# Kernel tuning notes

Measured on AMD Instinct MI355X. Metric: run time of the kernel, lower is better.

The kernel has to match this reference:

```python
import jax, jax.numpy as jnp
from jax import lax
import numpy as np

B, T, V, U = 64, 2048, 256, 256
BLANK = 0
NEG = jnp.float32(-1e30)


def setup_inputs() -> dict:
    key = jax.random.key(0)
    k1, k2, k3, k4 = jax.random.split(key, 4)
    logits = jax.random.normal(k1, (B, T, V), dtype=jnp.float32)
    targets = jax.random.randint(k2, (B, U), 1, V)               # labels 1..V-1 (0 = blank)
    targets_lengths = jax.random.randint(k3, (B,), U // 2, U + 1)
    logits_lengths = jax.random.randint(k4, (B,), T // 2, T + 1)
    return dict(logits=logits, targets=targets,
                logits_lengths=logits_lengths, targets_lengths=targets_lengths)


def _ctc_forced_alignment(logp, targets, logits_lengths, targets_lengths):
    """Viterbi forced alignment over the CTC extended state graph.
    Returns per-frame best-path labels, shape [B, T] (get_alignment_3d, is_ctc=True)."""
    Bs, Ts, _ = logp.shape
    Us = targets.shape[1]
    S = 2 * Us + 1
    s_idx = jnp.arange(S)
    # extended sequence: blank, t1, blank, t2, ..., blank
    lab_pos = jnp.minimum(s_idx // 2, Us - 1)
    ext = jnp.where((s_idx % 2 == 1)[None, :], jnp.take(targets, lab_pos, axis=1), BLANK)  # [B,S]
    # emission scores em[b,t,s] = logp[b,t,ext[b,s]]
    em = jnp.take_along_axis(logp, jnp.broadcast_to(ext[:, None, :], (Bs, Ts, S)), axis=2)

    valid = s_idx[None, :] < (2 * targets_lengths[:, None] + 1)              # [B,S]
    ext_m2 = jnp.pad(ext[:, :-2], ((0, 0), (2, 0)), constant_values=BLANK)
    skip_ok = (s_idx[None, :] >= 2) & ((s_idx % 2 == 1)[None, :]) & (ext != ext_m2)

    idx_blank = 2 * targets_lengths          # last blank state (S_b - 1)
    idx_label = 2 * targets_lengths - 1      # last label state (S_b - 2)

    alpha0 = jnp.where(valid & (s_idx[None, :] <= 1), em[:, 0, :], NEG)

    def pair_of(alpha):
        vb = jnp.take_along_axis(alpha, idx_blank[:, None], axis=1)
        vl = jnp.take_along_axis(alpha, idx_label[:, None], axis=1)
        return jnp.concatenate([vb, vl], axis=1)  # [B,2]

    def step(alpha, em_t):
        a1 = jnp.pad(alpha[:, :-1], ((0, 0), (1, 0)), constant_values=NEG)
        a2 = jnp.where(skip_ok, jnp.pad(alpha[:, :-2], ((0, 0), (2, 0)), constant_values=NEG), NEG)
        stacked = jnp.stack([alpha, a1, a2])     # [3,B,S]
        bp = jnp.argmax(stacked, axis=0).astype(jnp.int32)
        alpha_new = jnp.where(valid, jnp.max(stacked, axis=0) + em_t, NEG)
        return alpha_new, (bp, pair_of(alpha_new))

    _, (bps, pairs) = lax.scan(step, alpha0, jnp.moveaxis(em, 1, 0)[1:])
    bps = jnp.concatenate([jnp.zeros((1, Bs, S), jnp.int32), bps])            # [T,B,S]
    pairs = jnp.concatenate([pair_of(alpha0)[None], pairs])                   # [T,B,2]

    last_pair = pairs[logits_lengths - 1, jnp.arange(Bs)]                     # value at final valid frame
    end_state = jnp.where(last_pair[:, 0] >= last_pair[:, 1], idx_blank, idx_label).astype(jnp.int32)

    def back(s, inp):
        t, bp_t = inp
        label = jnp.take_along_axis(ext, s[:, None], axis=1)[:, 0]
        step_bp = jnp.take_along_axis(bp_t, s[:, None], axis=1)[:, 0]
        s_prev = jnp.where(t - 1 >= logits_lengths - 1, end_state, s - step_bp)
        return s_prev.astype(jnp.int32), label

    ts = jnp.arange(Ts - 1, -1, -1)
    _, labels_rev = lax.scan(back, end_state, (ts, bps[::-1]))
    return labels_rev[::-1].T  # [B,T] per-frame aligned target labels


def reference(logits, targets, logits_lengths, targets_lengths):
    logp = jax.nn.log_softmax(logits, axis=2)                                 # [B,T,V]
    aligned = lax.stop_gradient(
        _ctc_forced_alignment(logp, targets, logits_lengths, targets_lengths))
    nll = -jnp.take_along_axis(logp, aligned[:, :, None], axis=2)[..., 0]     # [B,T]
    mask = (jnp.arange(logp.shape[1])[None, :] < logits_lengths[:, None]).astype(logp.dtype)
    # reduce=True: mean over valid (unmasked) positions
    return jnp.sum(nll * mask) / jnp.sum(mask)
```

## Files before the change

kernel.cpp:

```cpp
#include <hip/hip_runtime.h>

#define NEGF -1e30f
typedef unsigned int uint32;

static constexpr int Bb = 64, Tt = 2048, Vv = 256, Uu = 256;

__device__ __forceinline__ unsigned short f2bf(float f) {
  uint32 u = __builtin_bit_cast(uint32, f);
  u += 0x7fffu + ((u >> 16) & 1u);
  return (unsigned short)(u >> 16);
}
__device__ __forceinline__ float bf2f_lo(uint32 p) { return __builtin_bit_cast(float, p << 16); }
__device__ __forceinline__ float bf2f_hi(uint32 p) { return __builtin_bit_cast(float, p & 0xffff0000u); }

__device__ __forceinline__ float dpp_shr1(float old, float src) {
  return __builtin_bit_cast(float, __builtin_amdgcn_update_dpp(
      __builtin_bit_cast(int, old), __builtin_bit_cast(int, src), 0x138, 0xF, 0xF, false));
}
__device__ __forceinline__ float dpp_shl1(float old, float src) {
  return __builtin_bit_cast(float, __builtin_amdgcn_update_dpp(
      __builtin_bit_cast(int, old), __builtin_bit_cast(int, src), 0x130, 0xF, 0xF, false));
}

__global__ __launch_bounds__(256) void gather_lse_kernel(
    const float* __restrict__ logits, const int* __restrict__ targets,
    const int* __restrict__ llen, float* __restrict__ acc,
    float* __restrict__ Ebs, unsigned short* __restrict__ E) {
  __shared__ __align__(16) float buf[4][8][Vv];
  __shared__ float wpart[4];
  const int b = blockIdx.x >> 5;
  const int c = blockIdx.x & 31;
  const int w = threadIdx.x >> 6;
  const int lane = threadIdx.x & 63;
  const int L = llen[b];
  const int4 lb = reinterpret_cast<const int4*>(targets + (b << 8))[lane];
  const float* __restrict__ lgb = logits + (size_t)b * (Tt * Vv);
  float lse_local = 0.f;
#pragma unroll
  for (int k = 0; k < 2; ++k) {
    const int tbase = (c << 6) + (k << 5) + w;
    if (tbase >= L) break;
    float4 v[8];
#pragma unroll
    for (int j = 0; j < 8; ++j)
      v[j] = reinterpret_cast<const float4*>(lgb + (size_t)(tbase + 4 * j) * Vv)[lane];
    float s[8];
#pragma unroll
    for (int j = 0; j < 8; ++j)
      s[j] = __expf(v[j].x) + __expf(v[j].y) + __expf(v[j].z) + __expf(v[j].w);
#pragma unroll
    for (int off = 32; off; off >>= 1) {
#pragma unroll
      for (int j = 0; j < 8; ++j) s[j] += __shfl_down(s[j], off);
    }
#pragma unroll
    for (int j = 0; j < 8; ++j)
      reinterpret_cast<float4*>(&buf[w][j][0])[lane] = v[j];
#pragma unroll
    for (int j = 0; j < 8; ++j) {
      const int t = tbase + 4 * j;
      const bool val = t < L;
      ushort4 o;
      o.x = f2bf(buf[w][j][lb.x]); o.y = f2bf(buf[w][j][lb.y]);
      o.z = f2bf(buf[w][j][lb.z]); o.w = f2bf(buf[w][j][lb.w]);
      if (val)
        reinterpret_cast<ushort4*>(E + ((size_t)((b << 11) + t)) * Vv)[lane] = o;
      if ((lane == 0) & val) {
        lse_local += __logf(s[j]);
        Ebs[(b << 11) + ((t == 0) ? 2047 : t - 1)] = v[j].x;
      }
    }
  }
  if (lane == 0) wpart[w] = lse_local;
  __syncthreads();
  if (threadIdx.x == 0)
    atomicAdd(acc, wpart[0] + wpart[1] + wpart[2] + wpart[3]);
}

#define PG 8
__global__ __launch_bounds__(128) void viterbi_kernel(
    const unsigned short* __restrict__ E, const float* __restrict__ Ebs,
    const int* __restrict__ targets, const int* __restrict__ llen,
    const int* __restrict__ tlen, float* __restrict__ acc) {
  __shared__ __align__(16) float LB[2048];
  __shared__ float Bt[520];
  const int b = blockIdx.x;
  const int lane = threadIdx.x & 63;
  const int wv = threadIdx.x >> 6;
  const int L = llen[b];
  const int tl = tlen[b];
  const int M = (L - 2) >> 1;
  const int4 lb = reinterpret_cast<const int4*>(targets + (b << 8))[lane];
  const uint2* __restrict__ Erow = reinterpret_cast<const uint2*>(E) + ((size_t)(b << 11) << 6);
  const float* __restrict__ Ebb = Ebs + (b << 11);

  {
    const float4* src = reinterpret_cast<const float4*>(Ebb);
    float4* dst = reinterpret_cast<float4*>(LB);
    for (int i = threadIdx.x; i < 512; i += 128) dst[i] = src[i];
  }
  __syncthreads();

  float a0 = NEGF, a1 = NEGF, a2 = NEGF, a3 = NEGF, a4 = NEGF,
        a5 = NEGF, a6 = NEGF, a7 = NEGF, a8 = NEGF;

  if (wv == 0) {
    const int prevw = __shfl_up(lb.w, 1);
    const bool sk0 = (lane != 0) && (lb.x != prevw);
    const bool sk1 = (lb.y != lb.x);
    const bool sk2 = (lb.z != lb.y);
    const bool sk3 = (lb.w != lb.z);
    if (lane == 0) {
      a0 = LB[2047];
      a1 = bf2f_lo((uint32)*reinterpret_cast<const unsigned short*>(E + ((size_t)(b << 11) << 8)));
    }
    uint2 pf[PG][4];
    float4 pb[PG];
    auto fetchf = [&](int slot, int k) {
      const int kk = (k > 511) ? 511 : k;
#pragma unroll
      for (int j = 0; j < 4; ++j) {
        int r = 1 + 4 * kk + j; r = (r > 2047) ? 2047 : r;
        pf[slot][j] = Erow[(size_t)(r << 6) + lane];
      }
      pb[slot] = reinterpret_cast<const float4*>(LB)[kk];
    };
    auto stepf = [&](uint2 em, float eb) {
      const float e0 = bf2f_lo(em.x), e1 = bf2f_hi(em.x);
      const float e2 = bf2f_lo(em.y), e3 = bf2f_hi(em.y);
      const float am1 = dpp_shr1(NEGF, a7);
      const float x0 = fmaxf(a0, am1) + eb;
      const float x1 = fmaxf(fmaxf(a1, a0), sk0 ? am1 : NEGF) + e0;
      const float x2 = fmaxf(a2, a1) + eb;
      const float x3 = fmaxf(fmaxf(a3, a2), sk1 ? a1 : NEGF) + e1;
      const float x4 = fmaxf(a4, a3) + eb;
      const float x5 = fmaxf(fmaxf(a5, a4), sk2 ? a3 : NEGF) + e2;
      const float x6 = fmaxf(a6, a5) + eb;
      const float x7 = fmaxf(fmaxf(a7, a6), sk3 ? a5 : NEGF) + e3;
      const float x8 = fmaxf(a8, a7) + eb;
      a0 = x0; a1 = x1; a2 = x2; a3 = x3; a4 = x4; a5 = x5; a6 = x6; a7 = x7; a8 = x8;
    };
    const int n = M, Gf = n >> 2, remf = n & 3;
#pragma unroll
    for (int s = 0; s < PG; ++s) fetchf(s, s);
    __builtin_amdgcn_sched_barrier(0);
    int g = 0;
    while (g + PG <= Gf) {
#pragma unroll
      for (int s = 0; s < PG; ++s) {
#pragma unroll
        for (int j = 0; j < 4; ++j) stepf(pf[s][j], (&pb[s].x)[j]);
        fetchf(s, g + s + PG);
        __builtin_amdgcn_sched_barrier(0);
      }
      g += PG;
    }
    const int left = Gf - g;
#pragma unroll
    for (int s = 0; s < PG; ++s) {
      if (s < left) {
#pragma unroll
        for (int j = 0; j < 4; ++j) stepf(pf[s][j], (&pb[s].x)[j]);
      }
    }
#pragma unroll
    for (int s = 0; s < PG; ++s) {
      if (s == left) {
#pragma unroll
        for (int j = 0; j < 4; ++j)
          if (j < remf) stepf(pf[s][j], (&pb[s].x)[j]);
      }
    }
  } else {
    const int nlabx = __shfl_down(lb.x, 1);
    const bool kb0 = (lb.y != lb.x);
    const bool kb1 = (lb.z != lb.y);
    const bool kb2 = (lb.w != lb.z);
    const bool kb3 = (lane < 63) && (nlabx != lb.w);
    {
      const uint2 er = Erow[(size_t)((L - 1) << 6) + lane];
      const float e0 = bf2f_lo(er.x), e1 = bf2f_hi(er.x);
      const float e2 = bf2f_lo(er.y), e3 = bf2f_hi(er.y);
      const float blankL = LB[L - 2];
      const int s0 = 8 * lane, tb = 2 * tl, tm = 2 * tl - 1;
      a0 = (s0     == tb) ? blankL : NEGF;
      a1 = (s0 + 1 == tm) ? e0     : NEGF;
      a2 = (s0 + 2 == tb) ? blankL : NEGF;
      a3 = (s0 + 3 == tm) ? e1     : NEGF;
      a4 = (s0 + 4 == tb) ? blankL : NEGF;
      a5 = (s0 + 5 == tm) ? e2     : NEGF;
      a6 = (s0 + 6 == tb) ? blankL : NEGF;
      a7 = (s0 + 7 == tm) ? e3     : NEGF;
      a8 = ((lane == 63) && (tb == 512)) ? blankL : NEGF;
    }
    uint2 qf[PG][4];
    float qb[PG][4];
    auto fetchb = [&](int slot, int k) {
#pragma unroll
      for (int j = 0; j < 4; ++j) {
        int r = L - 2 - 4 * k - j; r = (r < 1) ? 1 : r;
        qf[slot][j] = Erow[(size_t)(r << 6) + lane];
        qb[slot][j] = LB[r - 1];
      }
    };
    auto stepb = [&](uint2 em, float eb) {
      const float e0 = bf2f_lo(em.x), e1 = bf2f_hi(em.x);
      const float e2 = bf2f_lo(em.y), e3 = bf2f_hi(em.y);
      const float bn0 = dpp_shl1(a8, a0);
      const float bn1 = dpp_shl1(NEGF, a1);
      const float y0 = fmaxf(a0, a1) + eb;
      const float y1 = fmaxf(fmaxf(a1, a2), kb0 ? a3 : NEGF) + e0;
      const float y2 = fmaxf(a2, a3) + eb;
      const float y3 = fmaxf(fmaxf(a3, a4), kb1 ? a5 : NEGF) + e1;
      const float y4 = fmaxf(a4, a5) + eb;
      const float y5 = fmaxf(fmaxf(a5, a6), kb2 ? a7 : NEGF) + e2;
      const float y6 = fmaxf(a6, a7) + eb;
      const float y7 = fmaxf(fmaxf(a7, bn0), kb3 ? bn1 : NEGF) + e3;
      const float y8 = a8 + eb;
      a0 = y0; a1 = y1; a2 = y2; a3 = y3; a4 = y4; a5 = y5; a6 = y6; a7 = y7; a8 = y8;
    };
    const int n = L - 2 - M, Gb = n >> 2, remb = n & 3;
#pragma unroll
    for (int s = 0; s < PG; ++s) fetchb(s, s);
    __builtin_amdgcn_sched_barrier(0);
    int g = 0;
    while (g + PG <= Gb) {
#pragma unroll
      for (int s = 0; s < PG; ++s) {
#pragma unroll
        for (int j = 0; j < 4; ++j) stepb(qf[s][j], qb[s][j]);
        fetchb(s, g + s + PG);
        __builtin_amdgcn_sched_barrier(0);
      }
      g += PG;
    }
    const int left = Gb - g;
#pragma unroll
    for (int s = 0; s < PG; ++s) {
      if (s < left) {
#pragma unroll
        for (int j = 0; j < 4; ++j) stepb(qf[s][j], qb[s][j]);
      }
    }
#pragma unroll
    for (int s = 0; s < PG; ++s) {
      if (s == left) {
#pragma unroll
        for (int j = 0; j < 4; ++j)
          if (j < remb) stepb(qf[s][j], qb[s][j]);
      }
    }
    Bt[8 * lane + 0] = a0; Bt[8 * lane + 1] = a1;
    Bt[8 * lane + 2] = a2; Bt[8 * lane + 3] = a3;
    Bt[8 * lane + 4] = a4; Bt[8 * lane + 5] = a5;
    Bt[8 * lane + 6] = a6; Bt[8 * lane + 7] = a7;
    if (lane == 63) Bt[512] = a8;
    if (lane == 0) { Bt[513] = NEGF; Bt[514] = NEGF; }
  }
  __syncthreads();
  if (wv == 0) {
    const int nlabx = __shfl_down(lb.x, 1);
    const bool kb0 = (lb.y != lb.x);
    const bool kb1 = (lb.z != lb.y);
    const bool kb2 = (lb.w != lb.z);
    const bool kb3 = (lane < 63) && (nlabx != lb.w);
    const int s0 = 8 * lane;
    float best;
    best =             a0 + fmaxf(Bt[s0],     Bt[s0 + 1]);
    best = fmaxf(best, a1 + fmaxf(fmaxf(Bt[s0 + 1], Bt[s0 + 2]), kb0 ? Bt[s0 + 3] : NEGF));
    best = fmaxf(best, a2 + fmaxf(Bt[s0 + 2], Bt[s0 + 3]));
    best = fmaxf(best, a3 + fmaxf(fmaxf(Bt[s0 + 3], Bt[s0 + 4]), kb1 ? Bt[s0 + 5] : NEGF));
    best = fmaxf(best, a4 + fmaxf(Bt[s0 + 4], Bt[s0 + 5]));
    best = fmaxf(best, a5 + fmaxf(fmaxf(Bt[s0 + 5], Bt[s0 + 6]), kb2 ? Bt[s0 + 7] : NEGF));
    best = fmaxf(best, a6 + fmaxf(Bt[s0 + 6], Bt[s0 + 7]));
    best = fmaxf(best, a7 + fmaxf(fmaxf(Bt[s0 + 7], Bt[s0 + 8]), kb3 ? Bt[s0 + 9] : NEGF));
    best = fmaxf(best, a8 + Bt[512]);
#pragma unroll
    for (int off = 32; off; off >>= 1) best = fmaxf(best, __shfl_down(best, off));
    if (lane == 0) atomicAdd(acc, -best);
  }
}

__global__ __launch_bounds__(64) void finalize_kernel(
    const int* __restrict__ llen, const float* __restrict__ acc,
    float* __restrict__ out) {
  int Lsum = llen[threadIdx.x];
#pragma unroll
  for (int off = 32; off; off >>= 1) Lsum += __shfl_down(Lsum, off);
  if (threadIdx.x == 0) out[0] = acc[0] / (float)Lsum;
}

extern "C" void kernel_launch(void* const* d_in, const int* in_sizes, int n_in,
                              void* d_out, int out_size, void* d_ws, size_t ws_size,
                              hipStream_t stream) {
  const float* logits  = (const float*)d_in[0];
  const int*   targets = (const int*)d_in[1];
  const int*   llen    = (const int*)d_in[2];
  const int*   tlen    = (const int*)d_in[3];
  float* out = (float*)d_out;

  float*          acc = (float*)d_ws;
  float*          Ebs = (float*)((char*)d_ws + 4096);
  unsigned short* E   = (unsigned short*)((char*)d_ws + (1u << 20));

  hipMemsetAsync(acc, 0, 16, stream);
  gather_lse_kernel<<<Bb * 32, 256, 0, stream>>>(logits, targets, llen, acc, Ebs, E);
  viterbi_kernel<<<Bb, 128, 0, stream>>>(E, Ebs, targets, llen, tlen, acc);
  finalize_kernel<<<1, 64, 0, stream>>>(llen, acc, out);
}
```

Measured before the change: 278.5 us.

## Interleave forward and backward Viterbi passes in one wavefront

The viterbi kernel previously ran the forward and backward half-passes on two separate wavefronts of a 128-thread block. Now a single 64-lane wavefront runs both, interleaving their steps in one loop so the two independent dependency chains can hide each other's ALU and DPP latency. Prefetch depth is halved to keep register use in check, and tails are handled separately for each direction. The risk is higher register pressure and a loop that runs in series for the longer of the two halves, plus leftover steps outside the joint loop.

```diff
diff --git a/kernel.cpp b/kernel.cpp
--- a/kernel.cpp
+++ b/kernel.cpp
@@ -77,16 +77,15 @@
     atomicAdd(acc, wpart[0] + wpart[1] + wpart[2] + wpart[3]);
 }
 
-#define PG 8
-__global__ __launch_bounds__(128) void viterbi_kernel(
+#define PG 4
+__global__ __launch_bounds__(64) void viterbi_kernel(
     const unsigned short* __restrict__ E, const float* __restrict__ Ebs,
     const int* __restrict__ targets, const int* __restrict__ llen,
     const int* __restrict__ tlen, float* __restrict__ acc) {
   __shared__ __align__(16) float LB[2048];
   __shared__ float Bt[520];
   const int b = blockIdx.x;
-  const int lane = threadIdx.x & 63;
-  const int wv = threadIdx.x >> 6;
+  const int lane = threadIdx.x;
   const int L = llen[b];
   const int tl = tlen[b];
   const int M = (L - 2) >> 1;
@@ -97,184 +96,198 @@
   {
     const float4* src = reinterpret_cast<const float4*>(Ebb);
     float4* dst = reinterpret_cast<float4*>(LB);
-    for (int i = threadIdx.x; i < 512; i += 128) dst[i] = src[i];
+    for (int i = lane; i < 512; i += 64) dst[i] = src[i];
   }
   __syncthreads();
 
-  float a0 = NEGF, a1 = NEGF, a2 = NEGF, a3 = NEGF, a4 = NEGF,
-        a5 = NEGF, a6 = NEGF, a7 = NEGF, a8 = NEGF;
-
-  if (wv == 0) {
-    const int prevw = __shfl_up(lb.w, 1);
-    const bool sk0 = (lane != 0) && (lb.x != prevw);
-    const bool sk1 = (lb.y != lb.x);
-    const bool sk2 = (lb.z != lb.y);
-    const bool sk3 = (lb.w != lb.z);
-    if (lane == 0) {
-      a0 = LB[2047];
-      a1 = bf2f_lo((uint32)*reinterpret_cast<const unsigned short*>(E + ((size_t)(b << 11) << 8)));
-    }
-    uint2 pf[PG][4];
-    float4 pb[PG];
-    auto fetchf = [&](int slot, int k) {
-      const int kk = (k > 511) ? 511 : k;
+  const int prevw = __shfl_up(lb.w, 1);
+  const bool sk0 = (lane != 0) && (lb.x != prevw);
+  const bool sk1 = (lb.y != lb.x);
+  const bool sk2 = (lb.z != lb.y);
+  const bool sk3 = (lb.w != lb.z);
+  const int nlabx = __shfl_down(lb.x, 1);
+  const bool kb0 = sk1;
+  const bool kb1 = sk2;
+  const bool kb2 = sk3;
+  const bool kb3 = (lane < 63) && (nlabx != lb.w);
+
+  float f0 = NEGF, f1 = NEGF, f2 = NEGF, f3 = NEGF, f4 = NEGF,
+        f5 = NEGF, f6 = NEGF, f7 = NEGF, f8 = NEGF;
+  if (lane == 0) {
+    f0 = LB[2047];
+    f1 = bf2f_lo((uint32)*reinterpret_cast<const unsigned short*>(E + ((size_t)(b << 11) << 8)));
+  }
+
+  float h0, h1, h2, h3, h4, h5, h6, h7, h8;
+  {
+    const uint2 er = Erow[(size_t)((L - 1) << 6) + lane];
+    const float e0 = bf2f_lo(er.x), e1 = bf2f_hi(er.x);
+    const float e2 = bf2f_lo(er.y), e3 = bf2f_hi(er.y);
+    const float blankL = LB[L - 2];
+    const int s0 = 8 * lane, tb2 = 2 * tl, tm = 2 * tl - 1;
+    h0 = (s0     == tb2) ? blankL : NEGF;
+    h1 = (s0 + 1 == tm) ? e0     : NEGF;
+    h2 = (s0 + 2 == tb2) ? blankL : NEGF;
+    h3 = (s0 + 3 == tm) ? e1     : NEGF;
+    h4 = (s0 + 4 == tb2) ? blankL : NEGF;
+    h5 = (s0 + 5 == tm) ? e2     : NEGF;
+    h6 = (s0 + 6 == tb2) ? blankL : NEGF;
+    h7 = (s0 + 7 == tm) ? e3     : NEGF;
+    h8 = ((lane == 63) && (tb2 == 512)) ? blankL : NEGF;
+  }
+
+  uint2  pf[PG][4];  float4 pb4[PG];
+  uint2  qf[PG][4];  float  qb[PG][4];
+  auto fetchf = [&](int slot, int k) {
+    const int kk = (k > 511) ? 511 : k;
+#pragma unroll
+    for (int j = 0; j < 4; ++j) {
+      int r = 1 + 4 * kk + j; r = (r > 2047) ? 2047 : r;
+      pf[slot][j] = Erow[(size_t)(r << 6) + lane];
+    }
+    pb4[slot] = reinterpret_cast<const float4*>(LB)[kk];
+  };
+  auto fetchb = [&](int slot, int k) {
+#pragma unroll
+    for (int j = 0; j < 4; ++j) {
+      int r = L - 2 - 4 * k - j; r = (r < 1) ? 1 : r;
+      qf[slot][j] = Erow[(size_t)(r << 6) + lane];
+      qb[slot][j] = LB[r - 1];
+    }
+  };
+  auto stepf = [&](uint2 em, float eb) {
+    const float e0 = bf2f_lo(em.x), e1 = bf2f_hi(em.x);
+    const float e2 = bf2f_lo(em.y), e3 = bf2f_hi(em.y);
+    const float am1 = dpp_shr1(NEGF, f7);
+    const float x0 = fmaxf(f0, am1) + eb;
+    const float x1 = fmaxf(fmaxf(f1, f0), sk0 ? am1 : NEGF) + e0;
+    const float x2 = fmaxf(f2, f1) + eb;
+    const float x3 = fmaxf(fmaxf(f3, f2), sk1 ? f1 : NEGF) + e1;
+    const float x4 = fmaxf(f4, f3) + eb;
+    const float x5 = fmaxf(fmaxf(f5, f4), sk2 ? f3 : NEGF) + e2;
+    const float x6 = fmaxf(f6, f5) + eb;
+    const float x7 = fmaxf(fmaxf(f7, f6), sk3 ? f5 : NEGF) + e3;
+    const float x8 = fmaxf(f8, f7) + eb;
+    f0 = x0; f1 = x1; f2 = x2; f3 = x3; f4 = x4; f5 = x5; f6 = x6; f7 = x7; f8 = x8;
+  };
+  auto steph = [&](uint2 em, float eb) {
+    const float e0 = bf2f_lo(em.x), e1 = bf2f_hi(em.x);
+    const float e2 = bf2f_lo(em.y), e3 = bf2f_hi(em.y);
+    const float bn0 = dpp_shl1(h8, h0);
+    const float bn1 = dpp_shl1(NEGF, h1);
+    const float y0 = fmaxf(h0, h1) + eb;
+    const float y1 = fmaxf(fmaxf(h1, h2), kb0 ? h3 : NEGF) + e0;
+    const float y2 = fmaxf(h2, h3) + eb;
+    const float y3 = fmaxf(fmaxf(h3, h4), kb1 ? h5 : NEGF) + e1;
+    const float y4 = fmaxf(h4, h5) + eb;
+    const float y5 = fmaxf(fmaxf(h5, h6), kb2 ? h7 : NEGF) + e2;
+    const float y6 = fmaxf(h6, h7) + eb;
+    const float y7 = fmaxf(fmaxf(h7, bn0), kb3 ? bn1 : NEGF) + e3;
+    const float y8 = h8 + eb;
+    h0 = y0; h1 = y1; h2 = y2; h3 = y3; h4 = y4; h5 = y5; h6 = y6; h7 = y7; h8 = y8;
+  };
+
+  const int nf = M, nb = L - 2 - M;
+  const int Gf = nf >> 2, remf = nf & 3;
+  const int Gb = nb >> 2, remb = nb & 3;
+  const int Gmin = (Gf < Gb) ? Gf : Gb;
+
+#pragma unroll
+  for (int s = 0; s < PG; ++s) { fetchf(s, s); fetchb(s, s); }
+  __builtin_amdgcn_sched_barrier(0);
+
+  int g = 0;
+  while (g + PG <= Gmin) {
+#pragma unroll
+    for (int s = 0; s < PG; ++s) {
 #pragma unroll
       for (int j = 0; j < 4; ++j) {
-        int r = 1 + 4 * kk + j; r = (r > 2047) ? 2047 : r;
-        pf[slot][j] = Erow[(size_t)(r << 6) + lane];
-      }
-      pb[slot] = reinterpret_cast<const float4*>(LB)[kk];
-    };
-    auto stepf = [&](uint2 em, float eb) {
-      const float e0 = bf2f_lo(em.x), e1 = bf2f_hi(em.x);
-      const float e2 = bf2f_lo(em.y), e3 = bf2f_hi(em.y);
-      const float am1 = dpp_shr1(NEGF, a7);
-      const float x0 = fmaxf(a0, am1) + eb;
-      const float x1 = fmaxf(fmaxf(a1, a0), sk0 ? am1 : NEGF) + e0;
-      const float x2 = fmaxf(a2, a1) + eb;
-      const float x3 = fmaxf(fmaxf(a3, a2), sk1 ? a1 : NEGF) + e1;
-      const float x4 = fmaxf(a4, a3) + eb;
-      const float x5 = fmaxf(fmaxf(a5, a4), sk2 ? a3 : NEGF) + e2;
-      const float x6 = fmaxf(a6, a5) + eb;
-      const float x7 = fmaxf(fmaxf(a7, a6), sk3 ? a5 : NEGF) + e3;
-      const float x8 = fmaxf(a8, a7) + eb;
-      a0 = x0; a1 = x1; a2 = x2; a3 = x3; a4 = x4; a5 = x5; a6 = x6; a7 = x7; a8 = x8;
-    };
-    const int n = M, Gf = n >> 2, remf = n & 3;
-#pragma unroll
-    for (int s = 0; s < PG; ++s) fetchf(s, s);
-    __builtin_amdgcn_sched_barrier(0);
-    int g = 0;
-    while (g + PG <= Gf) {
+        stepf(pf[s][j], (&pb4[s].x)[j]);
+        steph(qf[s][j], qb[s][j]);
+      }
+      fetchf(s, g + s + PG);
+      fetchb(s, g + s + PG);
+      __builtin_amdgcn_sched_barrier(0);
+    }
+    g += PG;
+  }
+
+  {
+    const int leftf = Gf - g;
+#pragma unroll
+    for (int s = 0; s < PG; ++s) {
+      if (s < leftf) {
+#pragma unroll
+        for (int j = 0; j < 4; ++j) stepf(pf[s][j], (&pb4[s].x)[j]);
+      }
+    }
+    if (leftf == PG) {
+      if (remf) {
+        fetchf(0, g + PG);
+#pragma unroll
+        for (int j = 0; j < 4; ++j)
+          if (j < remf) stepf(pf[0][j], (&pb4[0].x)[j]);
+      }
+    } else {
 #pragma unroll
       for (int s = 0; s < PG; ++s) {
-#pragma unroll
-        for (int j = 0; j < 4; ++j) stepf(pf[s][j], (&pb[s].x)[j]);
-        fetchf(s, g + s + PG);
-        __builtin_amdgcn_sched_barrier(0);
-      }
-      g += PG;
-    }
-    const int left = Gf - g;
+        if (s == leftf) {
+#pragma unroll
+          for (int j = 0; j < 4; ++j)
+            if (j < remf) stepf(pf[s][j], (&pb4[s].x)[j]);
+        }
+      }
+    }
+  }
+
+  {
+    const int leftb = Gb - g;
 #pragma unroll
     for (int s = 0; s < PG; ++s) {
-      if (s < left) {
-#pragma unroll
-        for (int j = 0; j < 4; ++j) stepf(pf[s][j], (&pb[s].x)[j]);
-      }
-    }
-#pragma unroll
-    for (int s = 0; s < PG; ++s) {
-      if (s == left) {
+      if (s < leftb) {
+#pragma unroll
+        for (int j = 0; j < 4; ++j) steph(qf[s][j], qb[s][j]);
+      }
+    }
+    if (leftb == PG) {
+      if (remb) {
+        fetchb(0, g + PG);
 #pragma unroll
         for (int j = 0; j < 4; ++j)
-          if (j < remf) stepf(pf[s][j], (&pb[s].x)[j]);
-      }
-    }
-  } else {
-    const int nlabx = __shfl_down(lb.x, 1);
-    const bool kb0 = (lb.y != lb.x);
-    const bool kb1 = (lb.z != lb.y);
-    const bool kb2 = (lb.w != lb.z);
-    const bool kb3 = (lane < 63) && (nlabx != lb.w);
-    {
-      const uint2 er = Erow[(size_t)((L - 1) << 6) + lane];
-      const float e0 = bf2f_lo(er.x), e1 = bf2f_hi(er.x);
-      const float e2 = bf2f_lo(er.y), e3 = bf2f_hi(er.y);
-      const float blankL = LB[L - 2];
-      const int s0 = 8 * lane, tb = 2 * tl, tm = 2 * tl - 1;
-      a0 = (s0     == tb) ? blankL : NEGF;
-      a1 = (s0 + 1 == tm) ? e0     : NEGF;
-      a2 = (s0 + 2 == tb) ? blankL : NEGF;
-      a3 = (s0 + 3 == tm) ? e1     : NEGF;
-      a4 = (s0 + 4 == tb) ? blankL : NEGF;
-      a5 = (s0 + 5 == tm) ? e2     : NEGF;
-      a6 = (s0 + 6 == tb) ? blankL : NEGF;
-      a7 = (s0 + 7 == tm) ? e3     : NEGF;
-      a8 = ((lane == 63) && (tb == 512)) ? blankL : NEGF;
-    }
-    uint2 qf[PG][4];
-    float qb[PG][4];
-    auto fetchb = [&](int slot, int k) {
-#pragma unroll
-      for (int j = 0; j < 4; ++j) {
-        int r = L - 2 - 4 * k - j; r = (r < 1) ? 1 : r;
-        qf[slot][j] = Erow[(size_t)(r << 6) + lane];
-        qb[slot][j] = LB[r - 1];
-      }
-    };
-    auto stepb = [&](uint2 em, float eb) {
-      const float e0 = bf2f_lo(em.x), e1 = bf2f_hi(em.x);
-      const float e2 = bf2f_lo(em.y), e3 = bf2f_hi(em.y);
-      const float bn0 = dpp_shl1(a8, a0);
-      const float bn1 = dpp_shl1(NEGF, a1);
-      const float y0 = fmaxf(a0, a1) + eb;
-      const float y1 = fmaxf(fmaxf(a1, a2), kb0 ? a3 : NEGF) + e0;
-      const float y2 = fmaxf(a2, a3) + eb;
-      const float y3 = fmaxf(fmaxf(a3, a4), kb1 ? a5 : NEGF) + e1;
-      const float y4 = fmaxf(a4, a5) + eb;
-      const float y5 = fmaxf(fmaxf(a5, a6), kb2 ? a7 : NEGF) + e2;
-      const float y6 = fmaxf(a6, a7) + eb;
-      const float y7 = fmaxf(fmaxf(a7, bn0), kb3 ? bn1 : NEGF) + e3;
-      const float y8 = a8 + eb;
-      a0 = y0; a1 = y1; a2 = y2; a3 = y3; a4 = y4; a5 = y5; a6 = y6; a7 = y7; a8 = y8;
-    };
-    const int n = L - 2 - M, Gb = n >> 2, remb = n & 3;
-#pragma unroll
-    for (int s = 0; s < PG; ++s) fetchb(s, s);
-    __builtin_amdgcn_sched_barrier(0);
-    int g = 0;
-    while (g + PG <= Gb) {
+          if (j < remb) steph(qf[0][j], qb[0][j]);
+      }
+    } else {
 #pragma unroll
       for (int s = 0; s < PG; ++s) {
-#pragma unroll
-        for (int j = 0; j < 4; ++j) stepb(qf[s][j], qb[s][j]);
-        fetchb(s, g + s + PG);
-        __builtin_amdgcn_sched_barrier(0);
-      }
-      g += PG;
-    }
-    const int left = Gb - g;
-#pragma unroll
-    for (int s = 0; s < PG; ++s) {
-      if (s < left) {
-#pragma unroll
-        for (int j = 0; j < 4; ++j) stepb(qf[s][j], qb[s][j]);
-      }
-    }
-#pragma unroll
-    for (int s = 0; s < PG; ++s) {
-      if (s == left) {
-#pragma unroll
-        for (int j = 0; j < 4; ++j)
-          if (j < remb) stepb(qf[s][j], qb[s][j]);
-      }
-    }
-    Bt[8 * lane + 0] = a0; Bt[8 * lane + 1] = a1;
-    Bt[8 * lane + 2] = a2; Bt[8 * lane + 3] = a3;
-    Bt[8 * lane + 4] = a4; Bt[8 * lane + 5] = a5;
-    Bt[8 * lane + 6] = a6; Bt[8 * lane + 7] = a7;
-    if (lane == 63) Bt[512] = a8;
-    if (lane == 0) { Bt[513] = NEGF; Bt[514] = NEGF; }
-  }
+        if (s == leftb) {
+#pragma unroll
+          for (int j = 0; j < 4; ++j)
+            if (j < remb) steph(qf[s][j], qb[s][j]);
+        }
+      }
+    }
+  }
+
+  Bt[8 * lane + 0] = h0; Bt[8 * lane + 1] = h1;
+  Bt[8 * lane + 2] = h2; Bt[8 * lane + 3] = h3;
+  Bt[8 * lane + 4] = h4; Bt[8 * lane + 5] = h5;
+  Bt[8 * lane + 6] = h6; Bt[8 * lane + 7] = h7;
+  if (lane == 63) Bt[512] = h8;
+  if (lane == 0) { Bt[513] = NEGF; Bt[514] = NEGF; }
   __syncthreads();
-  if (wv == 0) {
-    const int nlabx = __shfl_down(lb.x, 1);
-    const bool kb0 = (lb.y != lb.x);
-    const bool kb1 = (lb.z != lb.y);
-    const bool kb2 = (lb.w != lb.z);
-    const bool kb3 = (lane < 63) && (nlabx != lb.w);
+
+  {
     const int s0 = 8 * lane;
     float best;
-    best =             a0 + fmaxf(Bt[s0],     Bt[s0 + 1]);
-    best = fmaxf(best, a1 + fmaxf(fmaxf(Bt[s0 + 1], Bt[s0 + 2]), kb0 ? Bt[s0 + 3] : NEGF));
-    best = fmaxf(best, a2 + fmaxf(Bt[s0 + 2], Bt[s0 + 3]));
-    best = fmaxf(best, a3 + fmaxf(fmaxf(Bt[s0 + 3], Bt[s0 + 4]), kb1 ? Bt[s0 + 5] : NEGF));
-    best = fmaxf(best, a4 + fmaxf(Bt[s0 + 4], Bt[s0 + 5]));
-    best = fmaxf(best, a5 + fmaxf(fmaxf(Bt[s0 + 5], Bt[s0 + 6]), kb2 ? Bt[s0 + 7] : NEGF));
-    best = fmaxf(best, a6 + fmaxf(Bt[s0 + 6], Bt[s0 + 7]));
-    best = fmaxf(best, a7 + fmaxf(fmaxf(Bt[s0 + 7], Bt[s0 + 8]), kb3 ? Bt[s0 + 9] : NEGF));
-    best = fmaxf(best, a8 + Bt[512]);
+    best =             f0 + fmaxf(Bt[s0],     Bt[s0 + 1]);
+    best = fmaxf(best, f1 + fmaxf(fmaxf(Bt[s0 + 1], Bt[s0 + 2]), kb0 ? Bt[s0 + 3] : NEGF));
+    best = fmaxf(best, f2 + fmaxf(Bt[s0 + 2], Bt[s0 + 3]));
+    best = fmaxf(best, f3 + fmaxf(fmaxf(Bt[s0 + 3], Bt[s0 + 4]), kb1 ? Bt[s0 + 5] : NEGF));
+    best = fmaxf(best, f4 + fmaxf(Bt[s0 + 4], Bt[s0 + 5]));
+    best = fmaxf(best, f5 + fmaxf(fmaxf(Bt[s0 + 5], Bt[s0 + 6]), kb2 ? Bt[s0 + 7] : NEGF));
+    best = fmaxf(best, f6 + fmaxf(Bt[s0 + 6], Bt[s0 + 7]));
+    best = fmaxf(best, f7 + fmaxf(fmaxf(Bt[s0 + 7], Bt[s0 + 8]), kb3 ? Bt[s0 + 9] : NEGF));
+    best = fmaxf(best, f8 + Bt[512]);
 #pragma unroll
     for (int off = 32; off; off >>= 1) best = fmaxf(best, __shfl_down(best, off));
     if (lane == 0) atomicAdd(acc, -best);
@@ -305,6 +318,6 @@
 
   hipMemsetAsync(acc, 0, 16, stream);
   gather_lse_kernel<<<Bb * 32, 256, 0, stream>>>(logits, targets, llen, acc, Ebs, E);
-  viterbi_kernel<<<Bb, 128, 0, stream>>>(E, Ebs, targets, llen, tlen, acc);
+  viterbi_kernel<<<Bb, 64, 0, stream>>>(E, Ebs, targets, llen, tlen, acc);
   finalize_kernel<<<1, 64, 0, stream>>>(llen, acc, out);
 }
```

New measurement: 340.2 us. 22.2% more time.

## Split Viterbi state range across two wavefronts per direction with wavefront-pipelined boundary exchange

Applied to the files above, without the earlier changes.

The forward and backward Viterbi passes each move from one wavefront owning 8 states per lane to two wavefronts owning 4 states per lane, one for the low half of the state range and one for the high half. The wave that depends on the other half's boundary column runs one phase of 64 frames behind, and boundary values pass through double-buffered shared memory at a barrier after each phase. This shortens the serial dependency chain per frame, roughly halving the per-step ALU work. In exchange it adds per-phase barriers, extra shared-memory traffic, and a one-phase pipeline fill delay.

```diff
diff --git a/kernel.cpp b/kernel.cpp
--- a/kernel.cpp
+++ b/kernel.cpp
@@ -77,208 +77,384 @@
     atomicAdd(acc, wpart[0] + wpart[1] + wpart[2] + wpart[3]);
 }
 
-#define PG 8
-__global__ __launch_bounds__(128) void viterbi_kernel(
+#define PG   4
+#define KCH  64
+#define GPP  16
+#define REVS 4
+
+__global__ __launch_bounds__(256, 1) void viterbi_kernel(
     const unsigned short* __restrict__ E, const float* __restrict__ Ebs,
     const int* __restrict__ targets, const int* __restrict__ llen,
     const int* __restrict__ tlen, float* __restrict__ acc) {
   __shared__ __align__(16) float LB[2048];
-  __shared__ float Bt[520];
+  __shared__ __align__(16) float Bf[2][KCH];
+  __shared__ __align__(16) float Bb0[2][KCH];
+  __shared__ __align__(16) float Bb1[2][KCH];
+  __shared__ __align__(16) float Bt[520];
+  __shared__ float Pm[2];
   const int b = blockIdx.x;
   const int lane = threadIdx.x & 63;
   const int wv = threadIdx.x >> 6;
   const int L = llen[b];
   const int tl = tlen[b];
   const int M = (L - 2) >> 1;
-  const int4 lb = reinterpret_cast<const int4*>(targets + (b << 8))[lane];
-  const uint2* __restrict__ Erow = reinterpret_cast<const uint2*>(E) + ((size_t)(b << 11) << 6);
+  const int nbl = L - 2 - M;
+  const int P = (nbl + KCH - 1) / KCH + 1;
+  const int hiw = (wv == 1 || wv == 2) ? 64 : 0;
+  const uint32* __restrict__ Er =
+      reinterpret_cast<const uint32*>(E) + ((size_t)b << 11) * 128 + hiw + lane;
   const float* __restrict__ Ebb = Ebs + (b << 11);
 
   {
     const float4* src = reinterpret_cast<const float4*>(Ebb);
     float4* dst = reinterpret_cast<float4*>(LB);
-    for (int i = threadIdx.x; i < 512; i += 128) dst[i] = src[i];
+    for (int i = threadIdx.x; i < 512; i += 256) dst[i] = src[i];
   }
   __syncthreads();
 
-  float a0 = NEGF, a1 = NEGF, a2 = NEGF, a3 = NEGF, a4 = NEGF,
-        a5 = NEGF, a6 = NEGF, a7 = NEGF, a8 = NEGF;
-
   if (wv == 0) {
-    const int prevw = __shfl_up(lb.w, 1);
-    const bool sk0 = (lane != 0) && (lb.x != prevw);
-    const bool sk1 = (lb.y != lb.x);
-    const bool sk2 = (lb.z != lb.y);
-    const bool sk3 = (lb.w != lb.z);
-    if (lane == 0) {
-      a0 = LB[2047];
-      a1 = bf2f_lo((uint32)*reinterpret_cast<const unsigned short*>(E + ((size_t)(b << 11) << 8)));
-    }
-    uint2 pf[PG][4];
-    float4 pb[PG];
-    auto fetchf = [&](int slot, int k) {
-      const int kk = (k > 511) ? 511 : k;
+    const int2 tt = reinterpret_cast<const int2*>(targets + (b << 8))[lane];
+    const int prev = __shfl_up(tt.y, 1);
+    const bool sk0 = (lane != 0) && (tt.x != prev);
+    const bool sk1 = (tt.y != tt.x);
+    float a0 = NEGF, a1 = NEGF, a2 = NEGF, a3 = NEGF;
+    if (lane == 0) { a0 = LB[2047]; a1 = bf2f_lo(Er[0]); }
+    uint32 pf[PG][4]; float4 pb[PG];
+    auto fetch = [&](int slot, int g) {
 #pragma unroll
       for (int j = 0; j < 4; ++j) {
-        int r = 1 + 4 * kk + j; r = (r > 2047) ? 2047 : r;
-        pf[slot][j] = Erow[(size_t)(r << 6) + lane];
-      }
+        int r = 1 + 4 * g + j; r = (r > 2047) ? 2047 : r;
+        pf[slot][j] = Er[(size_t)r * 128];
+      }
+      int kk = (g > 511) ? 511 : g;
       pb[slot] = reinterpret_cast<const float4*>(LB)[kk];
     };
-    auto stepf = [&](uint2 em, float eb) {
-      const float e0 = bf2f_lo(em.x), e1 = bf2f_hi(em.x);
-      const float e2 = bf2f_lo(em.y), e3 = bf2f_hi(em.y);
-      const float am1 = dpp_shr1(NEGF, a7);
+    auto step = [&](uint32 em, float eb) {
+      const float e0 = bf2f_lo(em), e1 = bf2f_hi(em);
+      const float am1 = dpp_shr1(NEGF, a3);
       const float x0 = fmaxf(a0, am1) + eb;
       const float x1 = fmaxf(fmaxf(a1, a0), sk0 ? am1 : NEGF) + e0;
       const float x2 = fmaxf(a2, a1) + eb;
       const float x3 = fmaxf(fmaxf(a3, a2), sk1 ? a1 : NEGF) + e1;
-      const float x4 = fmaxf(a4, a3) + eb;
-      const float x5 = fmaxf(fmaxf(a5, a4), sk2 ? a3 : NEGF) + e2;
-      const float x6 = fmaxf(a6, a5) + eb;
-      const float x7 = fmaxf(fmaxf(a7, a6), sk3 ? a5 : NEGF) + e3;
-      const float x8 = fmaxf(a8, a7) + eb;
-      a0 = x0; a1 = x1; a2 = x2; a3 = x3; a4 = x4; a5 = x5; a6 = x6; a7 = x7; a8 = x8;
-    };
-    const int n = M, Gf = n >> 2, remf = n & 3;
-#pragma unroll
-    for (int s = 0; s < PG; ++s) fetchf(s, s);
-    __builtin_amdgcn_sched_barrier(0);
-    int g = 0;
-    while (g + PG <= Gf) {
-#pragma unroll
-      for (int s = 0; s < PG; ++s) {
-#pragma unroll
-        for (int j = 0; j < 4; ++j) stepf(pf[s][j], (&pb[s].x)[j]);
-        fetchf(s, g + s + PG);
-        __builtin_amdgcn_sched_barrier(0);
-      }
-      g += PG;
-    }
-    const int left = Gf - g;
-#pragma unroll
-    for (int s = 0; s < PG; ++s) {
-      if (s < left) {
-#pragma unroll
-        for (int j = 0; j < 4; ++j) stepf(pf[s][j], (&pb[s].x)[j]);
-      }
-    }
-#pragma unroll
-    for (int s = 0; s < PG; ++s) {
-      if (s == left) {
-#pragma unroll
-        for (int j = 0; j < 4; ++j)
-          if (j < remf) stepf(pf[s][j], (&pb[s].x)[j]);
-      }
-    }
-  } else {
-    const int nlabx = __shfl_down(lb.x, 1);
-    const bool kb0 = (lb.y != lb.x);
-    const bool kb1 = (lb.z != lb.y);
-    const bool kb2 = (lb.w != lb.z);
-    const bool kb3 = (lane < 63) && (nlabx != lb.w);
-    {
-      const uint2 er = Erow[(size_t)((L - 1) << 6) + lane];
-      const float e0 = bf2f_lo(er.x), e1 = bf2f_hi(er.x);
-      const float e2 = bf2f_lo(er.y), e3 = bf2f_hi(er.y);
-      const float blankL = LB[L - 2];
-      const int s0 = 8 * lane, tb = 2 * tl, tm = 2 * tl - 1;
-      a0 = (s0     == tb) ? blankL : NEGF;
-      a1 = (s0 + 1 == tm) ? e0     : NEGF;
-      a2 = (s0 + 2 == tb) ? blankL : NEGF;
-      a3 = (s0 + 3 == tm) ? e1     : NEGF;
-      a4 = (s0 + 4 == tb) ? blankL : NEGF;
-      a5 = (s0 + 5 == tm) ? e2     : NEGF;
-      a6 = (s0 + 6 == tb) ? blankL : NEGF;
-      a7 = (s0 + 7 == tm) ? e3     : NEGF;
-      a8 = ((lane == 63) && (tb == 512)) ? blankL : NEGF;
-    }
-    uint2 qf[PG][4];
-    float qb[PG][4];
-    auto fetchb = [&](int slot, int k) {
-#pragma unroll
-      for (int j = 0; j < 4; ++j) {
-        int r = L - 2 - 4 * k - j; r = (r < 1) ? 1 : r;
-        qf[slot][j] = Erow[(size_t)(r << 6) + lane];
-        qb[slot][j] = LB[r - 1];
-      }
-    };
-    auto stepb = [&](uint2 em, float eb) {
-      const float e0 = bf2f_lo(em.x), e1 = bf2f_hi(em.x);
-      const float e2 = bf2f_lo(em.y), e3 = bf2f_hi(em.y);
-      const float bn0 = dpp_shl1(a8, a0);
-      const float bn1 = dpp_shl1(NEGF, a1);
-      const float y0 = fmaxf(a0, a1) + eb;
-      const float y1 = fmaxf(fmaxf(a1, a2), kb0 ? a3 : NEGF) + e0;
-      const float y2 = fmaxf(a2, a3) + eb;
-      const float y3 = fmaxf(fmaxf(a3, a4), kb1 ? a5 : NEGF) + e1;
-      const float y4 = fmaxf(a4, a5) + eb;
-      const float y5 = fmaxf(fmaxf(a5, a6), kb2 ? a7 : NEGF) + e2;
-      const float y6 = fmaxf(a6, a7) + eb;
-      const float y7 = fmaxf(fmaxf(a7, bn0), kb3 ? bn1 : NEGF) + e3;
-      const float y8 = a8 + eb;
-      a0 = y0; a1 = y1; a2 = y2; a3 = y3; a4 = y4; a5 = y5; a6 = y6; a7 = y7; a8 = y8;
-    };
-    const int n = L - 2 - M, Gb = n >> 2, remb = n & 3;
-#pragma unroll
-    for (int s = 0; s < PG; ++s) fetchb(s, s);
-    __builtin_amdgcn_sched_barrier(0);
-    int g = 0;
-    while (g + PG <= Gb) {
-#pragma unroll
-      for (int s = 0; s < PG; ++s) {
-#pragma unroll
-        for (int j = 0; j < 4; ++j) stepb(qf[s][j], qb[s][j]);
-        fetchb(s, g + s + PG);
-        __builtin_amdgcn_sched_barrier(0);
-      }
-      g += PG;
-    }
-    const int left = Gb - g;
-#pragma unroll
-    for (int s = 0; s < PG; ++s) {
-      if (s < left) {
-#pragma unroll
-        for (int j = 0; j < 4; ++j) stepb(qf[s][j], qb[s][j]);
-      }
-    }
-#pragma unroll
-    for (int s = 0; s < PG; ++s) {
-      if (s == left) {
-#pragma unroll
-        for (int j = 0; j < 4; ++j)
-          if (j < remb) stepb(qf[s][j], qb[s][j]);
-      }
-    }
-    Bt[8 * lane + 0] = a0; Bt[8 * lane + 1] = a1;
-    Bt[8 * lane + 2] = a2; Bt[8 * lane + 3] = a3;
-    Bt[8 * lane + 4] = a4; Bt[8 * lane + 5] = a5;
-    Bt[8 * lane + 6] = a6; Bt[8 * lane + 7] = a7;
-    if (lane == 63) Bt[512] = a8;
-    if (lane == 0) { Bt[513] = NEGF; Bt[514] = NEGF; }
-  }
-  __syncthreads();
-  if (wv == 0) {
-    const int nlabx = __shfl_down(lb.x, 1);
-    const bool kb0 = (lb.y != lb.x);
-    const bool kb1 = (lb.z != lb.y);
-    const bool kb2 = (lb.w != lb.z);
-    const bool kb3 = (lane < 63) && (nlabx != lb.w);
-    const int s0 = 8 * lane;
+      a0 = x0; a1 = x1; a2 = x2; a3 = x3;
+    };
+    const int n = M;
+#pragma unroll
+    for (int s = 0; s < PG; ++s) fetch(s, s);
+    __builtin_amdgcn_sched_barrier(0);
+    for (int p = 0; p < P; ++p) {
+      float* Bw = Bf[p & 1];
+      const int gbase = p * GPP;
+      for (int rev = 0; rev < REVS; ++rev) {
+#pragma unroll
+        for (int s = 0; s < PG; ++s) {
+          const int q = rev * PG + s;
+          const int g = gbase + q;
+          const int st0 = 4 * g;
+          if (st0 < n) {
+            float s0 = a3, s1, s2, s3;
+            if (st0 + 4 <= n) {
+              step(pf[s][0], pb[s].x); s1 = a3;
+              step(pf[s][1], pb[s].y); s2 = a3;
+              step(pf[s][2], pb[s].z); s3 = a3;
+              step(pf[s][3], pb[s].w);
+            } else {
+              const int rem = n - st0;
+              step(pf[s][0], pb[s].x); s1 = a3;
+              if (rem > 1) step(pf[s][1], pb[s].y); s2 = a3;
+              if (rem > 2) step(pf[s][2], pb[s].z); s3 = a3;
+            }
+            if (lane == 63) *reinterpret_cast<float4*>(&Bw[4 * q]) = make_float4(s0, s1, s2, s3);
+          }
+          fetch(s, g + PG);
+          __builtin_amdgcn_sched_barrier(0);
+        }
+      }
+      asm volatile("s_waitcnt lgkmcnt(0)" ::: "memory");
+      __builtin_amdgcn_sched_barrier(0);
+      __builtin_amdgcn_s_barrier();
+    }
+    asm volatile("s_waitcnt lgkmcnt(0)" ::: "memory");
+    __builtin_amdgcn_sched_barrier(0);
+    __builtin_amdgcn_s_barrier();
+    const int t128 = targets[(b << 8) + 128];
+    const int nx = __shfl_down(tt.x, 1);
+    const bool m1 = (lane == 63) ? (t128 != tt.y) : (nx != tt.y);
+    const int s0 = 4 * lane;
     float best;
     best =             a0 + fmaxf(Bt[s0],     Bt[s0 + 1]);
-    best = fmaxf(best, a1 + fmaxf(fmaxf(Bt[s0 + 1], Bt[s0 + 2]), kb0 ? Bt[s0 + 3] : NEGF));
+    best = fmaxf(best, a1 + fmaxf(fmaxf(Bt[s0 + 1], Bt[s0 + 2]), sk1 ? Bt[s0 + 3] : NEGF));
     best = fmaxf(best, a2 + fmaxf(Bt[s0 + 2], Bt[s0 + 3]));
-    best = fmaxf(best, a3 + fmaxf(fmaxf(Bt[s0 + 3], Bt[s0 + 4]), kb1 ? Bt[s0 + 5] : NEGF));
-    best = fmaxf(best, a4 + fmaxf(Bt[s0 + 4], Bt[s0 + 5]));
-    best = fmaxf(best, a5 + fmaxf(fmaxf(Bt[s0 + 5], Bt[s0 + 6]), kb2 ? Bt[s0 + 7] : NEGF));
-    best = fmaxf(best, a6 + fmaxf(Bt[s0 + 6], Bt[s0 + 7]));
-    best = fmaxf(best, a7 + fmaxf(fmaxf(Bt[s0 + 7], Bt[s0 + 8]), kb3 ? Bt[s0 + 9] : NEGF));
-    best = fmaxf(best, a8 + Bt[512]);
+    best = fmaxf(best, a3 + fmaxf(fmaxf(Bt[s0 + 3], Bt[s0 + 4]), m1 ? Bt[s0 + 5] : NEGF));
 #pragma unroll
     for (int off = 32; off; off >>= 1) best = fmaxf(best, __shfl_down(best, off));
-    if (lane == 0) atomicAdd(acc, -best);
+    if (lane == 0) Pm[0] = best;
+
+  } else if (wv == 1) {
+    const int2 tt = reinterpret_cast<const int2*>(targets + (b << 8))[64 + lane];
+    const int t127 = targets[(b << 8) + 127];
+    const int pw = __shfl_up(tt.y, 1);
+    const int prevh = (lane == 0) ? t127 : pw;
+    const bool skh0 = (tt.x != prevh);
+    const bool skh1 = (tt.y != tt.x);
+    float a0 = NEGF, a1 = NEGF, a2 = NEGF, a3 = NEGF, a4 = NEGF;
+    uint32 pf[PG][4]; float4 pb[PG];
+    auto fetch = [&](int slot, int g) {
+#pragma unroll
+      for (int j = 0; j < 4; ++j) {
+        int r = 1 + 4 * g + j; r = (r > 2047) ? 2047 : r;
+        pf[slot][j] = Er[(size_t)r * 128];
+      }
+      int kk = (g > 511) ? 511 : g;
+      pb[slot] = reinterpret_cast<const float4*>(LB)[kk];
+    };
+    auto step = [&](uint32 em, float eb, float bv) {
+      const float e0 = bf2f_lo(em), e1 = bf2f_hi(em);
+      const float am1 = dpp_shr1(bv, a3);
+      const float x0 = fmaxf(a0, am1) + eb;
+      const float x1 = fmaxf(fmaxf(a1, a0), skh0 ? am1 : NEGF) + e0;
+      const float x2 = fmaxf(a2, a1) + eb;
+      const float x3 = fmaxf(fmaxf(a3, a2), skh1 ? a1 : NEGF) + e1;
+      const float x4 = fmaxf(a4, a3) + eb;
+      a0 = x0; a1 = x1; a2 = x2; a3 = x3; a4 = x4;
+    };
+    const int n = M;
+#pragma unroll
+    for (int s = 0; s < PG; ++s) fetch(s, s);
+    __builtin_amdgcn_sched_barrier(0);
+    for (int p = 0; p < P; ++p) {
+      if (p >= 1) {
+        const float* Bw = Bf[(p - 1) & 1];
+        const int gbase = (p - 1) * GPP;
+        float4 bvA = reinterpret_cast<const float4*>(Bw)[0], bvB;
+        for (int rev = 0; rev < REVS; ++rev) {
+#pragma unroll
+          for (int s = 0; s < PG; ++s) {
+            const int q = rev * PG + s;
+            const int g = gbase + q;
+            const int st0 = 4 * g;
+            const int qn = (q < GPP - 1) ? (q + 1) : (GPP - 1);
+            float4 bv;
+            if (!(s & 1)) { bvB = reinterpret_cast<const float4*>(Bw)[qn]; bv = bvA; }
+            else          { bvA = reinterpret_cast<const float4*>(Bw)[qn]; bv = bvB; }
+            if (st0 < n) {
+              if (st0 + 4 <= n) {
+                step(pf[s][0], pb[s].x, bv.x);
+                step(pf[s][1], pb[s].y, bv.y);
+                step(pf[s][2], pb[s].z, bv.z);
+                step(pf[s][3], pb[s].w, bv.w);
+              } else {
+                const int rem = n - st0;
+                step(pf[s][0], pb[s].x, bv.x);
+                if (rem > 1) step(pf[s][1], pb[s].y, bv.y);
+                if (rem > 2) step(pf[s][2], pb[s].z, bv.z);
+              }
+            }
+            fetch(s, g + PG);
+            __builtin_amdgcn_sched_barrier(0);
+          }
+        }
+      }
+      asm volatile("s_waitcnt lgkmcnt(0)" ::: "memory");
+      __builtin_amdgcn_sched_barrier(0);
+      __builtin_amdgcn_s_barrier();
+    }
+    asm volatile("s_waitcnt lgkmcnt(0)" ::: "memory");
+    __builtin_amdgcn_sched_barrier(0);
+    __builtin_amdgcn_s_barrier();
+    const int nxh = __shfl_down(tt.x, 1);
+    const bool m1 = (lane < 63) && (nxh != tt.y);
+    const int s0 = 256 + 4 * lane;
+    float best;
+    best =             a0 + fmaxf(Bt[s0],     Bt[s0 + 1]);
+    best = fmaxf(best, a1 + fmaxf(fmaxf(Bt[s0 + 1], Bt[s0 + 2]), skh1 ? Bt[s0 + 3] : NEGF));
+    best = fmaxf(best, a2 + fmaxf(Bt[s0 + 2], Bt[s0 + 3]));
+    best = fmaxf(best, a3 + fmaxf(fmaxf(Bt[s0 + 3], Bt[s0 + 4]), m1 ? Bt[s0 + 5] : NEGF));
+    best = fmaxf(best, (lane == 63) ? (a4 + Bt[512]) : NEGF);
+#pragma unroll
+    for (int off = 32; off; off >>= 1) best = fmaxf(best, __shfl_down(best, off));
+    if (lane == 0) Pm[1] = best;
+
+  } else if (wv == 2) {
+    const int2 tt = reinterpret_cast<const int2*>(targets + (b << 8))[64 + lane];
+    const int nxh = __shfl_down(tt.x, 1);
+    const bool kb0 = (tt.y != tt.x);
+    const bool kb1 = (lane < 63) && (nxh != tt.y);
+    float h0, h1, h2, h3, h4;
+    {
+      const uint32 er = Er[(size_t)(L - 1) * 128];
+      const float e0 = bf2f_lo(er), e1 = bf2f_hi(er);
+      const float blankL = LB[L - 2];
+      const int s0h = 256 + 4 * lane, tb2 = 2 * tl, tm = 2 * tl - 1;
+      h0 = (s0h     == tb2) ? blankL : NEGF;
+      h1 = (s0h + 1 == tm ) ? e0     : NEGF;
+      h2 = (s0h + 2 == tb2) ? blankL : NEGF;
+      h3 = (s0h + 3 == tm ) ? e1     : NEGF;
+      h4 = ((lane == 63) && (tb2 == 512)) ? blankL : NEGF;
+    }
+    uint32 qf[PG][4]; float qb[PG][4];
+    auto fetch = [&](int slot, int g) {
+#pragma unroll
+      for (int j = 0; j < 4; ++j) {
+        int r = L - 2 - 4 * g - j; r = (r < 1) ? 1 : r;
+        qf[slot][j] = Er[(size_t)r * 128];
+        qb[slot][j] = LB[r - 1];
+      }
+    };
+    auto step = [&](uint32 em, float eb) {
+      const float e0 = bf2f_lo(em), e1 = bf2f_hi(em);
+      const float bn0 = dpp_shl1(h4, h0);
+      const float bn1 = dpp_shl1(NEGF, h1);
+      const float y0 = fmaxf(h0, h1) + eb;
+      const float y1 = fmaxf(fmaxf(h1, h2), kb0 ? h3 : NEGF) + e0;
+      const float y2 = fmaxf(h2, h3) + eb;
+      const float y3 = fmaxf(fmaxf(h3, bn0), kb1 ? bn1 : NEGF) + e1;
+      const float y4 = h4 + eb;
+      h0 = y0; h1 = y1; h2 = y2; h3 = y3; h4 = y4;
+    };
+    const int n = nbl;
+#pragma unroll
+    for (int s = 0; s < PG; ++s) fetch(s, s);
+    __builtin_amdgcn_sched_barrier(0);
+    for (int p = 0; p < P; ++p) {
+      float* Bw0 = Bb0[p & 1];
+      float* Bw1 = Bb1[p & 1];
+      const int gbase = p * GPP;
+      for (int rev = 0; rev < REVS; ++rev) {
+#pragma unroll
+        for (int s = 0; s < PG; ++s) {
+          const int q = rev * PG + s;
+          const int g = gbase + q;
+          const int st0 = 4 * g;
+          if (st0 < n) {
+            float u0 = h0, v0 = h1, u1, v1, u2, v2, u3, v3;
+            if (st0 + 4 <= n) {
+              step(qf[s][0], qb[s][0]); u1 = h0; v1 = h1;
+              step(qf[s][1], qb[s][1]); u2 = h0; v2 = h1;
+              step(qf[s][2], qb[s][2]); u3 = h0; v3 = h1;
+              step(qf[s][3], qb[s][3]);
+            } else {
+              const int rem = n - st0;
+              step(qf[s][0], qb[s][0]); u1 = h0; v1 = h1;
+              if (rem > 1) step(qf[s][1], qb[s][1]); u2 = h0; v2 = h1;
+              if (rem > 2) step(qf[s][2], qb[s][2]); u3 = h0; v3 = h1;
+            }
+            if (lane == 0) {
+              *reinterpret_cast<float4*>(&Bw0[4 * q]) = make_float4(u0, u1, u2, u3);
+              *reinterpret_cast<float4*>(&Bw1[4 * q]) = make_float4(v0, v1, v2, v3);
+            }
+          }
+          fetch(s, g + PG);
+          __builtin_amdgcn_sched_barrier(0);
+        }
+      }
+      asm volatile("s_waitcnt lgkmcnt(0)" ::: "memory");
+      __builtin_amdgcn_sched_barrier(0);
+      __builtin_amdgcn_s_barrier();
+    }
+    Bt[256 + 4 * lane + 0] = h0; Bt[256 + 4 * lane + 1] = h1;
+    Bt[256 + 4 * lane + 2] = h2; Bt[256 + 4 * lane + 3] = h3;
+    if (lane == 63) Bt[512] = h4;
+    if (lane == 0) { Bt[513] = NEGF; Bt[514] = NEGF; }
+    asm volatile("s_waitcnt lgkmcnt(0)" ::: "memory");
+    __builtin_amdgcn_sched_barrier(0);
+    __builtin_amdgcn_s_barrier();
+
+  } else {
+    const int2 tt = reinterpret_cast<const int2*>(targets + (b << 8))[lane];
+    const int t128 = targets[(b << 8) + 128];
+    const int nx = __shfl_down(tt.x, 1);
+    const bool kb0 = (tt.y != tt.x);
+    const bool kb1 = (lane == 63) ? (t128 != tt.y) : (nx != tt.y);
+    float h0, h1, h2, h3;
+    {
+      const uint32 er = Er[(size_t)(L - 1) * 128];
+      const float e0 = bf2f_lo(er), e1 = bf2f_hi(er);
+      const float blankL = LB[L - 2];
+      const int s0 = 4 * lane, tb2 = 2 * tl, tm = 2 * tl - 1;
+      h0 = (s0     == tb2) ? blankL : NEGF;
+      h1 = (s0 + 1 == tm ) ? e0     : NEGF;
+      h2 = (s0 + 2 == tb2) ? blankL : NEGF;
+      h3 = (s0 + 3 == tm ) ? e1     : NEGF;
+    }
+    uint32 qf[PG][4]; float qb[PG][4];
+    auto fetch = [&](int slot, int g) {
+#pragma unroll
+      for (int j = 0; j < 4; ++j) {
+        int r = L - 2 - 4 * g - j; r = (r < 1) ? 1 : r;
+        qf[slot][j] = Er[(size_t)r * 128];
+        qb[slot][j] = LB[r - 1];
+      }
+    };
+    auto step = [&](uint32 em, float eb, float bv0, float bv1) {
+      const float e0 = bf2f_lo(em), e1 = bf2f_hi(em);
+      const float bn0 = dpp_shl1(bv0, h0);
+      const float bn1 = dpp_shl1(bv1, h1);
+      const float y0 = fmaxf(h0, h1) + eb;
+      const float y1 = fmaxf(fmaxf(h1, h2), kb0 ? h3 : NEGF) + e0;
+      const float y2 = fmaxf(h2, h3) + eb;
+      const float y3 = fmaxf(fmaxf(h3, bn0), kb1 ? bn1 : NEGF) + e1;
+      h0 = y0; h1 = y1; h2 = y2; h3 = y3;
+    };
+    const int n = nbl;
+#pragma unroll
+    for (int s = 0; s < PG; ++s) fetch(s, s);
+    __builtin_amdgcn_sched_barrier(0);
+    for (int p = 0; p < P; ++p) {
+      if (p >= 1) {
+        const float* Bw0 = Bb0[(p - 1) & 1];
+        const float* Bw1 = Bb1[(p - 1) & 1];
+        const int gbase = (p - 1) * GPP;
+        float4 b0A = reinterpret_cast<const float4*>(Bw0)[0], b0B;
+        float4 b1A = reinterpret_cast<const float4*>(Bw1)[0], b1B;
+        for (int rev = 0; rev < REVS; ++rev) {
+#pragma unroll
+          for (int s = 0; s < PG; ++s) {
+            const int q = rev * PG + s;
+            const int g = gbase + q;
+            const int st0 = 4 * g;
+            const int qn = (q < GPP - 1) ? (q + 1) : (GPP - 1);
+            float4 c0, c1;
+            if (!(s & 1)) {
+              b0B = reinterpret_cast<const float4*>(Bw0)[qn];
+              b1B = reinterpret_cast<const float4*>(Bw1)[qn];
+              c0 = b0A; c1 = b1A;
+            } else {
+              b0A = reinterpret_cast<const float4*>(Bw0)[qn];
+              b1A = reinterpret_cast<const float4*>(Bw1)[qn];
+              c0 = b0B; c1 = b1B;
+            }
+            if (st0 < n) {
+              if (st0 + 4 <= n) {
+                step(qf[s][0], qb[s][0], c0.x, c1.x);
+                step(qf[s][1], qb[s][1], c0.y, c1.y);
+                step(qf[s][2], qb[s][2], c0.z, c1.z);
+                step(qf[s][3], qb[s][3], c0.w, c1.w);
+              } else {
+                const int rem = n - st0;
+                step(qf[s][0], qb[s][0], c0.x, c1.x);
+                if (rem > 1) step(qf[s][1], qb[s][1], c0.y, c1.y);
+                if (rem > 2) step(qf[s][2], qb[s][2], c0.z, c1.z);
+              }
+            }
+            fetch(s, g + PG);
+            __builtin_amdgcn_sched_barrier(0);
+          }
+        }
+      }
+      asm volatile("s_waitcnt lgkmcnt(0)" ::: "memory");
+      __builtin_amdgcn_sched_barrier(0);
+      __builtin_amdgcn_s_barrier();
+    }
+    Bt[4 * lane + 0] = h0; Bt[4 * lane + 1] = h1;
+    Bt[4 * lane + 2] = h2; Bt[4 * lane + 3] = h3;
+    asm volatile("s_waitcnt lgkmcnt(0)" ::: "memory");
+    __builtin_amdgcn_sched_barrier(0);
+    __builtin_amdgcn_s_barrier();
   }
+
+  __syncthreads();
+  if (threadIdx.x == 0) atomicAdd(acc, -fmaxf(Pm[0], Pm[1]));
 }
 
 __global__ __launch_bounds__(64) void finalize_kernel(
@@ -305,6 +481,6 @@
 
   hipMemsetAsync(acc, 0, 16, stream);
   gather_lse_kernel<<<Bb * 32, 256, 0, stream>>>(logits, targets, llen, acc, Ebs, E);
-  viterbi_kernel<<<Bb, 128, 0, stream>>>(E, Ebs, targets, llen, tlen, acc);
+  viterbi_kernel<<<Bb, 256, 0, stream>>>(E, Ebs, targets, llen, tlen, acc);
   finalize_kernel<<<1, 64, 0, stream>>>(llen, acc, out);
 }
```

New measurement: 288.2 us. +3.5%, slower.
